# Performance work log

Measured on AMD Instinct MI355X. Metric: run time of the kernel, lower is better.

## Reference

```python
import jax, jax.numpy as jnp
import numpy as np

CORR_THRESHOLD = 0.3
EPS = 1e-8


def setup_inputs() -> dict:
    key = jax.random.key(0)
    x = jax.random.normal(key, (128, 8192, 64), dtype=jnp.float32)  # [B, W, D]
    return {"x": x}


def reference(x) -> jnp.ndarray:
    # x: [B, W, D]. Per-batch Pearson correlation matrix via one batched GEMM
    # (mathematically equal to the per-feature zero-lag FFT cross-correlation
    # loop in the original forward, fused into bwi,bwj).
    B, W, D = x.shape
    centered = x - jnp.mean(x, axis=1, keepdims=True)            # [B, W, D]
    cov = jnp.einsum('bwi,bwj->bij', centered, centered) / (W - 1)  # [B, D, D]
    std = jnp.sqrt(jnp.diagonal(cov, axis1=1, axis2=2)) + EPS    # [B, D] (unbiased std, matches torch.std)
    corr = cov / (std[:, :, None] * std[:, None, :])             # [B, D, D]
    significant = (jnp.abs(corr) > CORR_THRESHOLD).astype(x.dtype)
    # self-correlation is always 1 > threshold, so subtract 1
    return jnp.sum(significant, axis=2) - 1.0                    # [B, D]
```

## Files before the change

### kernel.cpp

```cpp
#include <hip/hip_runtime.h>
#include <stdint.h>

#define BATCH 128
#define W_LEN 8192
#define D_FEAT 64
#define WC 128
#define LDS_STRIDE 68
#define LDSU (D_FEAT * LDS_STRIDE)
#define WS_PER_SLICE 4160

typedef __bf16 bf16x8 __attribute__((ext_vector_type(8)));
typedef float f32x4 __attribute__((ext_vector_type(4)));

union FragU { uint4 u; bf16x8 v; };

__device__ __forceinline__ unsigned int pack_bf16_pair(float a, float b) {
  return __builtin_amdgcn_perm(__float_as_uint(b), __float_as_uint(a), 0x07060302u);
}

__global__ void __launch_bounds__(256, 4)
cov_partial_kernel(const float* __restrict__ x, float* __restrict__ ws, int S) {
  __shared__ __align__(16) unsigned int lds_u[2][LDSU];
  __shared__ float ssum_scratch[256 * 4];
  const int tid  = threadIdx.x;
  const int lane = tid & 63;
  const int wid  = tid >> 6;
  const int s = blockIdx.x;
  const int b = blockIdx.y;
  const int ws_per  = W_LEN / S;
  const int nchunks = ws_per / WC;

  const int q = tid & 15;
  const int T = tid >> 4;
  const int m  = lane & 15;
  const int hi = lane >> 4;

  f32x4 acc[4];
  #pragma unroll
  for (int t = 0; t < 4; t++)
    #pragma unroll
    for (int r = 0; r < 4; r++) acc[t][r] = 0.0f;

  float ssum[4] = {0.f, 0.f, 0.f, 0.f};

  const size_t base = ((size_t)b * W_LEN + (size_t)s * ws_per) * D_FEAT;
  const float* src0 = x + base + (size_t)(8 * T) * D_FEAT + 4 * q;

  float4 ld[8];
  #pragma unroll
  for (int r = 0; r < 8; r++) ld[r] = *(const float4*)(src0 + r * D_FEAT);

  for (int c = 0; c < nchunks; c++) {
    unsigned int* buf = lds_u[c & 1];
    #pragma unroll
    for (int j = 0; j < 4; j++) {
      const float* f0 = (const float*)&ld[0];
      uint4 pk;
      pk.x = pack_bf16_pair(f0[0 * 4 + j], f0[1 * 4 + j]);
      pk.y = pack_bf16_pair(f0[2 * 4 + j], f0[3 * 4 + j]);
      pk.z = pack_bf16_pair(f0[4 * 4 + j], f0[5 * 4 + j]);
      pk.w = pack_bf16_pair(f0[6 * 4 + j], f0[7 * 4 + j]);
      ssum[j] += ((f0[0 * 4 + j] + f0[1 * 4 + j]) + (f0[2 * 4 + j] + f0[3 * 4 + j]))
               + ((f0[4 * 4 + j] + f0[5 * 4 + j]) + (f0[6 * 4 + j] + f0[7 * 4 + j]));
      *(uint4*)&buf[(4 * q + j) * LDS_STRIDE + 4 * T] = pk;
    }
    if (c + 1 < nchunks) {
      const float* srcn = src0 + (size_t)(c + 1) * WC * D_FEAT;
      #pragma unroll
      for (int r = 0; r < 8; r++) ld[r] = *(const float4*)(srcn + r * D_FEAT);
    }
    __syncthreads();
    #pragma unroll
    for (int st = 0; st < 4; st++) {
      const int ko = st * 16 + hi * 4;
      FragU fA;
      fA.u = *(const uint4*)&buf[(16 * wid + m) * LDS_STRIDE + ko];
      #pragma unroll
      for (int t = 0; t < 4; t++) {
        FragU fB;
        fB.u = *(const uint4*)&buf[(16 * t + m) * LDS_STRIDE + ko];
        acc[t] = __builtin_amdgcn_mfma_f32_16x16x32_bf16(fA.v, fB.v, acc[t], 0, 0, 0);
      }
    }
  }

  float* out_base = ws + (size_t)(b * S + s) * WS_PER_SLICE;
  #pragma unroll
  for (int t = 0; t < 4; t++)
    #pragma unroll
    for (int r = 0; r < 4; r++) {
      const int row = 16 * wid + hi * 4 + r;
      const int col = 16 * t + m;
      out_base[row * D_FEAT + col] = acc[t][r];
    }

  #pragma unroll
  for (int j = 0; j < 4; j++) ssum_scratch[tid * 4 + j] = ssum[j];
  __syncthreads();
  if (tid < D_FEAT) {
    const int qq = tid >> 2, jj = tid & 3;
    float t = 0.f;
    #pragma unroll
    for (int g = 0; g < 16; g++) t += ssum_scratch[(g * 16 + qq) * 4 + jj];
    out_base[4096 + tid] = t;
  }
}

__global__ void __launch_bounds__(256)
corr_count_kernel(const float* __restrict__ ws, float* __restrict__ out, int S) {
  __shared__ __align__(16) float cov[4096];
  __shared__ float sums[D_FEAT];
  __shared__ float rstd[D_FEAT];
  __shared__ float cnts[256];
  const int tid = threadIdx.x;
  const int b = blockIdx.x;
  const float* base = ws + (size_t)b * S * WS_PER_SLICE;

  #pragma unroll
  for (int it = 0; it < 4; it++) {
    const int idx = (it * 256 + tid) * 4;
    float ax = 0.f, ay = 0.f, az = 0.f, aw = 0.f;
    for (int s = 0; s < S; s++) {
      float4 v = *(const float4*)&base[(size_t)s * WS_PER_SLICE + idx];
      ax += v.x; ay += v.y; az += v.z; aw += v.w;
    }
    float4 a; a.x = ax; a.y = ay; a.z = az; a.w = aw;
    *(float4*)&cov[idx] = a;
  }
  if (tid < D_FEAT) {
    float t = 0.f;
    for (int s = 0; s < S; s++) t += base[(size_t)s * WS_PER_SLICE + 4096 + tid];
    sums[tid] = t;
  }
  __syncthreads();
  if (tid < D_FEAT) {
    const float sd = sums[tid];
    float c = (cov[tid * D_FEAT + tid] - sd * sd * (1.0f / W_LEN)) * (1.0f / (W_LEN - 1));
    c = c > 0.f ? c : 0.f;
    rstd[tid] = 1.0f / (sqrtf(c) + 1e-8f);
  }
  __syncthreads();
  {
    const int r = tid >> 2, part = tid & 3;
    const float sr = sums[r];
    const float rs_r = rstd[r];
    float cnt = 0.f;
    #pragma unroll
    for (int k = 0; k < 16; k++) {
      const int cc = part * 16 + k;
      const float cv = (cov[r * D_FEAT + cc] - sr * sums[cc] * (1.0f / W_LEN)) * (1.0f / (W_LEN - 1));
      const float corr = cv * rs_r * rstd[cc];
      cnt += (fabsf(corr) > 0.3f) ? 1.0f : 0.0f;
    }
    cnts[tid] = cnt;
  }
  __syncthreads();
  if (tid < D_FEAT) {
    const float t = cnts[tid * 4] + cnts[tid * 4 + 1] + cnts[tid * 4 + 2] + cnts[tid * 4 + 3];
    out[(size_t)b * D_FEAT + tid] = t - 1.0f;
  }
}

extern "C" void kernel_launch(void* const* d_in, const int* in_sizes, int n_in,
                              void* d_out, int out_size, void* d_ws, size_t ws_size,
                              hipStream_t stream) {
  const float* x = (const float*)d_in[0];
  float* out = (float*)d_out;
  float* ws  = (float*)d_ws;

  int S = 8;
  while (S > 1 && (size_t)BATCH * S * WS_PER_SLICE * sizeof(float) > ws_size) S >>= 1;

  dim3 g1(S, BATCH);
  cov_partial_kernel<<<g1, 256, 0, stream>>>(x, ws, S);
  corr_count_kernel<<<BATCH, 256, 0, stream>>>(ws, out, S);
}
```

Measured before the change: 367.7 us.

## Compute column sums via MFMA with ones and split reduction kernel per half-batch

Column sums are now produced by one extra bf16 MFMA per k-step against a ones vector, replacing the scalar fp32 adds and the shared-memory reduction at the end. This changes the sums to bf16-rounded inputs, which matches the bf16 rounding of the cross-product terms. The second kernel is templated on S so its loops fully unroll, and it is split into two blocks per batch that each handle 32 rows, doubling its parallelism. Diagonal entries are read separately so that each block only loads its half of the covariance.

Result: faster. 359.2 us (-2.3%).

```diff
diff --git a/kernel.cpp b/kernel.cpp
--- a/kernel.cpp
+++ b/kernel.cpp
@@ -21,7 +21,6 @@
 __global__ void __launch_bounds__(256, 4)
 cov_partial_kernel(const float* __restrict__ x, float* __restrict__ ws, int S) {
   __shared__ __align__(16) unsigned int lds_u[2][LDSU];
-  __shared__ float ssum_scratch[256 * 4];
   const int tid  = threadIdx.x;
   const int lane = tid & 63;
   const int wid  = tid >> 6;
@@ -41,7 +40,13 @@
     #pragma unroll
     for (int r = 0; r < 4; r++) acc[t][r] = 0.0f;
 
-  float ssum[4] = {0.f, 0.f, 0.f, 0.f};
+  f32x4 accs;
+  #pragma unroll
+  for (int r = 0; r < 4; r++) accs[r] = 0.0f;
+
+  FragU ones;
+  ones.u.x = 0x3F803F80u; ones.u.y = 0x3F803F80u;
+  ones.u.z = 0x3F803F80u; ones.u.w = 0x3F803F80u;
 
   const size_t base = ((size_t)b * W_LEN + (size_t)s * ws_per) * D_FEAT;
   const float* src0 = x + base + (size_t)(8 * T) * D_FEAT + 4 * q;
@@ -60,8 +65,6 @@
       pk.y = pack_bf16_pair(f0[2 * 4 + j], f0[3 * 4 + j]);
       pk.z = pack_bf16_pair(f0[4 * 4 + j], f0[5 * 4 + j]);
       pk.w = pack_bf16_pair(f0[6 * 4 + j], f0[7 * 4 + j]);
-      ssum[j] += ((f0[0 * 4 + j] + f0[1 * 4 + j]) + (f0[2 * 4 + j] + f0[3 * 4 + j]))
-               + ((f0[4 * 4 + j] + f0[5 * 4 + j]) + (f0[6 * 4 + j] + f0[7 * 4 + j]));
       *(uint4*)&buf[(4 * q + j) * LDS_STRIDE + 4 * T] = pk;
     }
     if (c + 1 < nchunks) {
@@ -81,6 +84,7 @@
         fB.u = *(const uint4*)&buf[(16 * t + m) * LDS_STRIDE + ko];
         acc[t] = __builtin_amdgcn_mfma_f32_16x16x32_bf16(fA.v, fB.v, acc[t], 0, 0, 0);
       }
+      accs = __builtin_amdgcn_mfma_f32_16x16x32_bf16(fA.v, ones.v, accs, 0, 0, 0);
     }
   }
 
@@ -94,70 +98,80 @@
       out_base[row * D_FEAT + col] = acc[t][r];
     }
 
-  #pragma unroll
-  for (int j = 0; j < 4; j++) ssum_scratch[tid * 4 + j] = ssum[j];
-  __syncthreads();
-  if (tid < D_FEAT) {
-    const int qq = tid >> 2, jj = tid & 3;
-    float t = 0.f;
+  if (m == 0) {
     #pragma unroll
-    for (int g = 0; g < 16; g++) t += ssum_scratch[(g * 16 + qq) * 4 + jj];
-    out_base[4096 + tid] = t;
+    for (int r = 0; r < 4; r++)
+      out_base[4096 + 16 * wid + hi * 4 + r] = accs[r];
   }
 }
 
+template<int S>
 __global__ void __launch_bounds__(256)
-corr_count_kernel(const float* __restrict__ ws, float* __restrict__ out, int S) {
-  __shared__ __align__(16) float cov[4096];
+corr_count_kernel_t(const float* __restrict__ ws, float* __restrict__ out) {
+  __shared__ __align__(16) float covh[2048];
   __shared__ float sums[D_FEAT];
+  __shared__ float diagv[D_FEAT];
   __shared__ float rstd[D_FEAT];
   __shared__ float cnts[256];
-  const int tid = threadIdx.x;
-  const int b = blockIdx.x;
+  const int tid  = threadIdx.x;
+  const int b    = blockIdx.x >> 1;
+  const int half = blockIdx.x & 1;
+  const int rowbase = half * 32;
   const float* base = ws + (size_t)b * S * WS_PER_SLICE;
 
   #pragma unroll
-  for (int it = 0; it < 4; it++) {
-    const int idx = (it * 256 + tid) * 4;
+  for (int it = 0; it < 2; it++) {
+    const int lidx = (it * 256 + tid) * 4;
     float ax = 0.f, ay = 0.f, az = 0.f, aw = 0.f;
+    #pragma unroll
     for (int s = 0; s < S; s++) {
-      float4 v = *(const float4*)&base[(size_t)s * WS_PER_SLICE + idx];
+      float4 v = *(const float4*)&base[(size_t)s * WS_PER_SLICE + rowbase * D_FEAT + lidx];
       ax += v.x; ay += v.y; az += v.z; aw += v.w;
     }
     float4 a; a.x = ax; a.y = ay; a.z = az; a.w = aw;
-    *(float4*)&cov[idx] = a;
+    *(float4*)&covh[lidx] = a;
   }
   if (tid < D_FEAT) {
     float t = 0.f;
+    #pragma unroll
     for (int s = 0; s < S; s++) t += base[(size_t)s * WS_PER_SLICE + 4096 + tid];
     sums[tid] = t;
+  } else if (tid < 2 * D_FEAT) {
+    const int d = tid - D_FEAT;
+    float t = 0.f;
+    #pragma unroll
+    for (int s = 0; s < S; s++) t += base[(size_t)s * WS_PER_SLICE + d * (D_FEAT + 1)];
+    diagv[d] = t;
   }
   __syncthreads();
   if (tid < D_FEAT) {
     const float sd = sums[tid];
-    float c = (cov[tid * D_FEAT + tid] - sd * sd * (1.0f / W_LEN)) * (1.0f / (W_LEN - 1));
+    float c = (diagv[tid] - sd * sd * (1.0f / W_LEN)) * (1.0f / (W_LEN - 1));
     c = c > 0.f ? c : 0.f;
     rstd[tid] = 1.0f / (sqrtf(c) + 1e-8f);
   }
   __syncthreads();
   {
-    const int r = tid >> 2, part = tid & 3;
-    const float sr = sums[r];
-    const float rs_r = rstd[r];
+    const int r = tid >> 3;
+    const int part = tid & 7;
+    const float sr  = sums[rowbase + r];
+    const float rs_r = rstd[rowbase + r];
     float cnt = 0.f;
     #pragma unroll
-    for (int k = 0; k < 16; k++) {
-      const int cc = part * 16 + k;
-      const float cv = (cov[r * D_FEAT + cc] - sr * sums[cc] * (1.0f / W_LEN)) * (1.0f / (W_LEN - 1));
+    for (int k = 0; k < 8; k++) {
+      const int cc = part * 8 + k;
+      const float cv = (covh[r * D_FEAT + cc] - sr * sums[cc] * (1.0f / W_LEN)) * (1.0f / (W_LEN - 1));
       const float corr = cv * rs_r * rstd[cc];
       cnt += (fabsf(corr) > 0.3f) ? 1.0f : 0.0f;
     }
     cnts[tid] = cnt;
   }
   __syncthreads();
-  if (tid < D_FEAT) {
-    const float t = cnts[tid * 4] + cnts[tid * 4 + 1] + cnts[tid * 4 + 2] + cnts[tid * 4 + 3];
-    out[(size_t)b * D_FEAT + tid] = t - 1.0f;
+  if (tid < 32) {
+    float t = 0.f;
+    #pragma unroll
+    for (int k = 0; k < 8; k++) t += cnts[tid * 8 + k];
+    out[(size_t)b * D_FEAT + rowbase + tid] = t - 1.0f;
   }
 }
 
@@ -173,5 +187,12 @@
 
   dim3 g1(S, BATCH);
   cov_partial_kernel<<<g1, 256, 0, stream>>>(x, ws, S);
-  corr_count_kernel<<<BATCH, 256, 0, stream>>>(ws, out, S);
+
+  dim3 g2(BATCH * 2);
+  switch (S) {
+    case 8: corr_count_kernel_t<8><<<g2, 256, 0, stream>>>(ws, out); break;
+    case 4: corr_count_kernel_t<4><<<g2, 256, 0, stream>>>(ws, out); break;
+    case 2: corr_count_kernel_t<2><<<g2, 256, 0, stream>>>(ws, out); break;
+    default: corr_count_kernel_t<1><<<g2, 256, 0, stream>>>(ws, out); break;
+  }
 }
```
